# Performance work log

Measured on AMD Instinct MI355X. Metric: run time of the kernel, lower is better.

Reference implementation:

```python
import jax, jax.numpy as jnp
import numpy as np

EPS = 1e-5


def _bn_relu(h, gamma, beta):
    # BatchNorm1d in training mode: stats over all but the last (channel) dim
    m = h.reshape(-1, h.shape[-1])
    mu = jnp.mean(m, axis=0)
    var = jnp.var(m, axis=0)
    return jax.nn.relu((h - mu) * jax.lax.rsqrt(var + EPS) * gamma + beta)


def setup_inputs() -> dict:
    key = jax.random.key(0)
    ks = jax.random.split(key, 16)
    B, N, D, OUT = 64, 64, 64, 128
    T = 2 * D          # object_tuple_size = 128
    HG, HF = 256, 128  # hidden_dim_g, hidden_dim_f

    def lin(k, i, o):
        return (jax.random.normal(k, (i, o), jnp.float32) / np.sqrt(i).astype(np.float32),
                jnp.zeros((o,), jnp.float32))

    inp = {"x": jax.random.normal(ks[0], (B, N, D), jnp.float32)}
    # G: depth-3 Linear-BN-ReLU, dims T -> HG -> HG -> T
    for i, (a, b) in enumerate([(T, HG), (HG, HG), (HG, T)]):
        W, bb = lin(ks[1 + i], a, b)
        inp[f"gW{i}"] = W
        inp[f"gb{i}"] = bb
        inp[f"gg{i}"] = jnp.ones((b,), jnp.float32)
        inp[f"gB{i}"] = jnp.zeros((b,), jnp.float32)
    # F: depth-2 Linear-BN-ReLU, dims T -> HF -> T, then Linear(T, OUT)
    for i, (a, b) in enumerate([(T, HF), (HF, T)]):
        W, bb = lin(ks[5 + i], a, b)
        inp[f"fW{i}"] = W
        inp[f"fb{i}"] = bb
        inp[f"fg{i}"] = jnp.ones((b,), jnp.float32)
        inp[f"fB{i}"] = jnp.zeros((b,), jnp.float32)
    inp["foW"], inp["fob"] = lin(ks[8], T, OUT)
    return inp


def reference(x, gW0, gb0, gg0, gB0, gW1, gb1, gg1, gB1, gW2, gb2, gg2, gB2,
              fW0, fb0, fg0, fB0, fW1, fb1, fg1, fB1, foW, fob):
    B, N, D = x.shape
    # GroupObjectsIntoPairs: all ordered pairs -> (B, N*N, 2D)
    xi = jnp.broadcast_to(x[:, :, None, :], (B, N, N, D))
    xj = jnp.broadcast_to(x[:, None, :, :], (B, N, N, D))
    h = jnp.concatenate([xi, xj], axis=-1).reshape(B, N * N, 2 * D)
    # G: per-pair MLP
    for W, b, g, be in ((gW0, gb0, gg0, gB0), (gW1, gb1, gg1, gB1), (gW2, gb2, gg2, gB2)):
        h = _bn_relu(h @ W + b, g, be)
    # sum over pair dimension (no layer norm)
    s = h.sum(axis=1)  # (B, 2D)
    # F: MLP + final linear
    for W, b, g, be in ((fW0, fb0, fg0, fB0), (fW1, fb1, fg1, fB1)):
        s = _bn_relu(s @ W + b, g, be)
    return s @ foW + fob  # (B, OUT)
```

## Files before the change

### kernel.cpp

```cpp
#include <hip/hip_runtime.h>


typedef _Float16 half8 __attribute__((ext_vector_type(8)));
typedef _Float16 half4_t __attribute__((ext_vector_type(4)));
typedef float float4_t __attribute__((ext_vector_type(4)));

static constexpr float kEps = 1e-5f;
static constexpr float kM = 262144.f;

static constexpr size_t OFF_U   = 0;
static constexpr size_t OFF_V   = OFF_U  + (size_t)4096*256*4;
static constexpr size_t OFF_UP  = OFF_V  + (size_t)4096*256*4;
static constexpr size_t OFF_VP  = OFF_UP + (size_t)4096*256*2;
static constexpr size_t OFF_W1T = OFF_VP + (size_t)4096*256*2;
static constexpr size_t OFF_W2T = OFF_W1T + (size_t)256*256*2;
static constexpr size_t OFF_Z1  = OFF_W2T + (size_t)128*256*2;
static constexpr size_t OFF_ST0 = OFF_Z1 + (size_t)262144*256*2;
static constexpr size_t OFF_C0S = OFF_ST0 + (size_t)64*4*256*4;
static constexpr size_t OFF_C0T = OFF_C0S + 1024;
static constexpr size_t OFF_C1S = OFF_C0T + 1024;
static constexpr size_t OFF_C1T = OFF_C1S + 1024;
static constexpr size_t OFF_C2S = OFF_C1T + 1024;
static constexpr size_t OFF_C2T = OFF_C2S + 512;
static constexpr size_t OFF_ST1 = OFF_C2T + 512;
static constexpr size_t OFF_ST2 = OFF_ST1 + (size_t)32*512*4;
static constexpr size_t OFF_SB  = OFF_ST2 + (size_t)32*256*4;
static constexpr size_t OFF_FST0 = OFF_SB + (size_t)64*128*4;
static constexpr size_t OFF_FST1 = OFF_FST0 + 1024;
static constexpr size_t ZERO_BYTES = (size_t)32*512*4 + (size_t)32*256*4
                                   + (size_t)64*128*4 + 2048;
static constexpr size_t OFF_FZ0  = OFF_FST1 + 1024;
static constexpr size_t OFF_FZ1  = OFF_FZ0 + (size_t)64*128*4;
static constexpr size_t OFF_CF0S = OFF_FZ1 + (size_t)64*128*4;
static constexpr size_t OFF_CF0T = OFF_CF0S + 512;
static constexpr size_t OFF_CF1S = OFF_CF0T + 512;
static constexpr size_t OFF_CF1T = OFF_CF1S + 512;
static constexpr size_t OFF_C1H  = OFF_CF1T + 512;
static constexpr size_t OFF_Z2   = OFF_C1H + 1024;
static constexpr size_t WS_REQUIRED = OFF_Z2 + (size_t)262144*128*2;

static __device__ inline half8 relu8(half8 s) {
#pragma unroll
  for (int e = 0; e < 8; ++e) s[e] = s[e] > (_Float16)0 ? s[e] : (_Float16)0;
  return s;
}

__global__ __launch_bounds__(256) void k_wt(const float* __restrict__ gW1,
                                            const float* __restrict__ gW2,
                                            _Float16* __restrict__ W1T,
                                            _Float16* __restrict__ W2T) {
  int idx = blockIdx.x * 256 + threadIdx.x;
  if (idx < 65536) {
    int n = idx >> 8, k = idx & 255;
    W1T[idx] = (_Float16)gW1[k * 256 + n];
  } else if (idx < 98304) {
    int j = idx - 65536;
    int n = j >> 8, k = j & 255;
    W2T[j] = (_Float16)gW2[k * 128 + n];
  }
}

__global__ __launch_bounds__(256) void k_prep(const float* __restrict__ x,
                                              const float* __restrict__ gW0,
                                              float* __restrict__ U,
                                              float* __restrict__ V) {
  __shared__ __align__(16) float sX[32 * 64];
  int t = threadIdx.x;
  int p0 = blockIdx.x * 32;
  int by = blockIdx.y;
  int hsel = by >> 1;
  int cbase = (by & 1) * 128;
#pragma unroll
  for (int it = 0; it < 2; ++it) {
    int f4 = (it * 256 + t) * 4;
    *(float4_t*)(sX + f4) = *(const float4_t*)(x + (size_t)p0 * 64 + f4);
  }
  __syncthreads();
  int r = t >> 3, cg = (t & 7) * 16;
  const float* Wb = gW0 + (size_t)(hsel * 64) * 256 + cbase + cg;
  float acc[16];
#pragma unroll
  for (int j = 0; j < 16; ++j) acc[j] = 0.f;
  for (int k = 0; k < 64; ++k) {
    float xv = sX[r * 64 + k];
    const float4_t* wr = (const float4_t*)(Wb + (size_t)k * 256);
    float4_t w0 = wr[0], w1 = wr[1], w2 = wr[2], w3 = wr[3];
#pragma unroll
    for (int j = 0; j < 4; ++j) {
      acc[j]      += xv * w0[j];
      acc[4 + j]  += xv * w1[j];
      acc[8 + j]  += xv * w2[j];
      acc[12 + j] += xv * w3[j];
    }
  }
  float* outp = (hsel ? V : U) + (size_t)(p0 + r) * 256 + cbase + cg;
#pragma unroll
  for (int q = 0; q < 4; ++q) {
    float4_t o = {acc[q * 4], acc[q * 4 + 1], acc[q * 4 + 2], acc[q * 4 + 3]};
    *(float4_t*)(outp + q * 4) = o;
  }
}

__global__ __launch_bounds__(256) void k_stats0(const float* __restrict__ U,
                                                const float* __restrict__ V,
                                                float* __restrict__ st0) {
  int b = blockIdx.x, c = threadIdx.x;
  float su = 0, su2 = 0, sv = 0, sv2 = 0;
  for (int i = 0; i < 64; ++i) {
    float u = U[(size_t)(b * 64 + i) * 256 + c];
    float v = V[(size_t)(b * 64 + i) * 256 + c];
    su += u; su2 += u * u; sv += v; sv2 += v * v;
  }
  st0[(b * 4 + 0) * 256 + c] = su;
  st0[(b * 4 + 1) * 256 + c] = su2;
  st0[(b * 4 + 2) * 256 + c] = sv;
  st0[(b * 4 + 3) * 256 + c] = sv2;
}

__global__ __launch_bounds__(256) void k_bn0(const float* __restrict__ st0,
                                             const float* __restrict__ gb0,
                                             const float* __restrict__ gg0,
                                             const float* __restrict__ gB0,
                                             float* __restrict__ c0s,
                                             float* __restrict__ c0t) {
  int c = threadIdx.x;
  float su = 0, su2 = 0, sv = 0, sv2 = 0, cross = 0;
  for (int b = 0; b < 64; ++b) {
    float a  = st0[(b * 4 + 0) * 256 + c];
    float a2 = st0[(b * 4 + 1) * 256 + c];
    float v  = st0[(b * 4 + 2) * 256 + c];
    float v2 = st0[(b * 4 + 3) * 256 + c];
    su += a; su2 += a2; sv += v; sv2 += v2; cross += a * v;
  }
  float b0 = gb0[c];
  float sumz  = 64.f * (su + sv) + kM * b0;
  float sumzz = 64.f * (su2 + sv2) + 2.f * cross + 2.f * b0 * 64.f * (su + sv) + kM * b0 * b0;
  float mu = sumz / kM;
  float var = sumzz / kM - mu * mu;
  float sc = gg0[c] * rsqrtf(var + kEps);
  c0s[c] = sc;
  c0t[c] = gB0[c] + sc * (b0 - mu);
}

__global__ __launch_bounds__(256) void k_uv(const float* __restrict__ U,
                                            const float* __restrict__ V,
                                            const float* __restrict__ c0s,
                                            const float* __restrict__ c0t,
                                            _Float16* __restrict__ Up,
                                            _Float16* __restrict__ Vp) {
  int idx = blockIdx.x * 256 + threadIdx.x;
  int e4 = idx * 4;
  int c4 = e4 & 255;
  float4_t u = *(const float4_t*)(U + e4);
  float4_t v = *(const float4_t*)(V + e4);
  float4_t s = *(const float4_t*)(c0s + c4);
  float4_t tt = *(const float4_t*)(c0t + c4);
  half4_t hu, hv;
#pragma unroll
  for (int e = 0; e < 4; ++e) {
    hu[e] = (_Float16)(u[e] * s[e] + tt[e]);
    hv[e] = (_Float16)(v[e] * s[e]);
  }
  *(half4_t*)(Up + e4) = hu;
  *(half4_t*)(Vp + e4) = hv;
}

__global__ __launch_bounds__(256) void k_gemm1(const _Float16* __restrict__ Up,
                                               const _Float16* __restrict__ Vp,
                                               const _Float16* __restrict__ W1T,
                                               const float* __restrict__ gb1,
                                               _Float16* __restrict__ Z1,
                                               float* __restrict__ stats1) {
  __shared__ __align__(16) char smem[2 * 128 * 72 * 2];
  _Float16* sA = (_Float16*)smem;
  _Float16* sW = (_Float16*)(smem + 128 * 72 * 2);
  _Float16* sO = (_Float16*)smem;

  const int t = threadIdx.x;
  const int bx = blockIdx.x;
  const int n0 = blockIdx.y * 128;
  const int b = bx >> 5;
  const int i0 = (bx & 31) * 2;
  const long R0 = (long)bx * 128;

  const int wid = t >> 6, L = t & 63;
  const int wrow = wid >> 1, wcol = wid & 1;
  const int quad = L >> 4, l15 = L & 15;

  const int prow = t >> 2;
  const int pk = (t & 3) * 16;

  const _Float16* UpI0 = Up + (size_t)(b * 64 + i0) * 256;
  const _Float16* UpI1 = UpI0 + 256;
  const _Float16* VpJ  = Vp + (size_t)(b * 64 + prow) * 256;

  float4_t acc[4][4];
#pragma unroll
  for (int mt = 0; mt < 4; ++mt)
#pragma unroll
    for (int nt = 0; nt < 4; ++nt) acc[mt][nt] = (float4_t){0.f, 0.f, 0.f, 0.f};

  for (int kc = 0; kc < 4; ++kc) {
    __syncthreads();
    {
      const int kg = kc * 64 + pk;
      half8 va = *(const half8*)(VpJ + kg);
      half8 vb = *(const half8*)(VpJ + kg + 8);
      half8 u0a = *(const half8*)(UpI0 + kg);
      half8 u0b = *(const half8*)(UpI0 + kg + 8);
      half8 u1a = *(const half8*)(UpI1 + kg);
      half8 u1b = *(const half8*)(UpI1 + kg + 8);
      *(half8*)(sA + prow * 72 + pk)            = relu8(u0a + va);
      *(half8*)(sA + prow * 72 + pk + 8)        = relu8(u0b + vb);
      *(half8*)(sA + (64 + prow) * 72 + pk)     = relu8(u1a + va);
      *(half8*)(sA + (64 + prow) * 72 + pk + 8) = relu8(u1b + vb);
    }
#pragma unroll
    for (int it = 0; it < 4; ++it) {
      int flat = it * 256 + t;
      int row = flat >> 3, c8 = (flat & 7) * 8;
      *(half8*)(sW + row * 72 + c8) =
          *(const half8*)(W1T + (size_t)(n0 + row) * 256 + kc * 64 + c8);
    }
    __syncthreads();
#pragma unroll
    for (int ks = 0; ks < 2; ++ks) {
      const int kk = ks * 32 + quad * 8;
      half8 afr[4];
#pragma unroll
      for (int mt = 0; mt < 4; ++mt)
        afr[mt] = *(const half8*)(sA + (wrow * 64 + mt * 16 + l15) * 72 + kk);
      half8 bfr[4];
#pragma unroll
      for (int nt = 0; nt < 4; ++nt)
        bfr[nt] = *(const half8*)(sW + (wcol * 64 + nt * 16 + l15) * 72 + kk);
#pragma unroll
      for (int mt = 0; mt < 4; ++mt)
#pragma unroll
        for (int nt = 0; nt < 4; ++nt)
          acc[mt][nt] = __builtin_amdgcn_mfma_f32_16x16x32_f16(afr[mt], bfr[nt],
                                                               acc[mt][nt], 0, 0, 0);
    }
  }

  __syncthreads();
  const int rep = bx & 31;
#pragma unroll
  for (int nt = 0; nt < 4; ++nt) {
    const int lcol = wcol * 64 + nt * 16 + l15;
    const float b1c = gb1[n0 + lcol];
    float sz = 0.f, szz = 0.f;
#pragma unroll
    for (int mt = 0; mt < 4; ++mt) {
      const int lrow = wrow * 64 + mt * 16 + quad * 4;
#pragma unroll
      for (int r = 0; r < 4; ++r) {
        float z = acc[mt][nt][r] + b1c;
        sO[(lrow + r) * 136 + lcol] = (_Float16)z;
        sz += z;
        szz += z * z;
      }
    }
    sz += __shfl_xor(sz, 16, 64);
    sz += __shfl_xor(sz, 32, 64);
    szz += __shfl_xor(szz, 16, 64);
    szz += __shfl_xor(szz, 32, 64);
    if (quad == 0) {
      atomicAdd(stats1 + rep * 512 + n0 + lcol, sz);
      atomicAdd(stats1 + rep * 512 + 256 + n0 + lcol, szz);
    }
  }
  __syncthreads();
#pragma unroll
  for (int it = 0; it < 8; ++it) {
    int cid = it * 256 + t;
    int row = cid >> 4, ch = (cid & 15) * 8;
    half8 hv = *(const half8*)(sO + row * 136 + ch);
    *(half8*)(Z1 + (size_t)(R0 + row) * 256 + n0 + ch) = hv;
  }
}

__global__ __launch_bounds__(256) void k_bn1(const float* __restrict__ stats1,
                                             const float* __restrict__ gg1,
                                             const float* __restrict__ gB1,
                                             float* __restrict__ c1s,
                                             float* __restrict__ c1t,
                                             _Float16* __restrict__ c1h) {
  int c = threadIdx.x;
  float S = 0.f, S2 = 0.f;
  for (int rp = 0; rp < 32; ++rp) {
    S += stats1[rp * 512 + c];
    S2 += stats1[rp * 512 + 256 + c];
  }
  float mu = S / kM;
  float var = S2 / kM - mu * mu;
  float sc = gg1[c] * rsqrtf(var + kEps);
  float sh = gB1[c] - sc * mu;
  c1s[c] = sc;
  c1t[c] = sh;
  c1h[c] = (_Float16)sc;
  c1h[256 + c] = (_Float16)sh;
}

__global__ __launch_bounds__(256) void k_gemm2(const _Float16* __restrict__ Z1,
                                               const _Float16* __restrict__ W2T,
                                               const _Float16* __restrict__ c1h,
                                               const float* __restrict__ gb2,
                                               _Float16* __restrict__ Z2,
                                               float* __restrict__ stats2) {
  __shared__ __align__(16) char smem[2 * 128 * 72 * 2];
  _Float16* sA = (_Float16*)smem;
  _Float16* sW = (_Float16*)(smem + 128 * 72 * 2);
  _Float16* sO = (_Float16*)smem;
  __shared__ __align__(16) _Float16 sSh[256];
  __shared__ __align__(16) _Float16 sTh[256];
  const int t = threadIdx.x;
  const int bx = blockIdx.x;
  const long R0 = (long)bx * 128;
  sSh[t] = c1h[t];
  sTh[t] = c1h[256 + t];

  const int wid = t >> 6, L = t & 63;
  const int wrow = wid >> 1, wcol = wid & 1;
  const int quad = L >> 4, l15 = L & 15;

  float4_t acc[4][4];
#pragma unroll
  for (int mt = 0; mt < 4; ++mt)
#pragma unroll
    for (int nt = 0; nt < 4; ++nt) acc[mt][nt] = (float4_t){0.f, 0.f, 0.f, 0.f};

  for (int kc = 0; kc < 4; ++kc) {
    __syncthreads();
#pragma unroll
    for (int it = 0; it < 2; ++it) {
      int flat = it * 256 + t;
      int row = flat >> 3, k8 = (flat & 7) * 8;
      int kg = kc * 64 + k8;
      half8 hv = *(const half8*)(Z1 + ((size_t)R0 + row) * 256 + kg);
      half8 hs = *(const half8*)(sSh + kg);
      half8 ht = *(const half8*)(sTh + kg);
      half8 ov = relu8(hv * hs + ht);
      *(half8*)(sA + row * 72 + k8) = ov;
      int row2 = row + 64;
      half8 hv2 = *(const half8*)(Z1 + ((size_t)R0 + row2) * 256 + kg);
      half8 ov2 = relu8(hv2 * hs + ht);
      *(half8*)(sA + row2 * 72 + k8) = ov2;
    }
#pragma unroll
    for (int it = 0; it < 4; ++it) {
      int flat = it * 256 + t;
      int row = flat >> 3, k8 = (flat & 7) * 8;
      *(half8*)(sW + row * 72 + k8) =
          *(const half8*)(W2T + (size_t)row * 256 + kc * 64 + k8);
    }
    __syncthreads();
#pragma unroll
    for (int ks = 0; ks < 2; ++ks) {
      const int kk = ks * 32 + quad * 8;
      half8 afr[4];
#pragma unroll
      for (int mt = 0; mt < 4; ++mt)
        afr[mt] = *(const half8*)(sA + (wrow * 64 + mt * 16 + l15) * 72 + kk);
      half8 bfr[4];
#pragma unroll
      for (int nt = 0; nt < 4; ++nt)
        bfr[nt] = *(const half8*)(sW + (wcol * 64 + nt * 16 + l15) * 72 + kk);
#pragma unroll
      for (int mt = 0; mt < 4; ++mt)
#pragma unroll
        for (int nt = 0; nt < 4; ++nt)
          acc[mt][nt] = __builtin_amdgcn_mfma_f32_16x16x32_f16(afr[mt], bfr[nt],
                                                               acc[mt][nt], 0, 0, 0);
    }
  }

  __syncthreads();
  const int rep = bx & 31;
#pragma unroll
  for (int nt = 0; nt < 4; ++nt) {
    const int lcol = wcol * 64 + nt * 16 + l15;
    const float b2c = gb2[lcol];
    float sz = 0.f, szz = 0.f;
#pragma unroll
    for (int mt = 0; mt < 4; ++mt) {
      const int lrow = wrow * 64 + mt * 16 + quad * 4;
#pragma unroll
      for (int r = 0; r < 4; ++r) {
        float z = acc[mt][nt][r] + b2c;
        sO[(lrow + r) * 136 + lcol] = (_Float16)z;
        sz += z;
        szz += z * z;
      }
    }
    sz += __shfl_xor(sz, 16, 64);
    sz += __shfl_xor(sz, 32, 64);
    szz += __shfl_xor(szz, 16, 64);
    szz += __shfl_xor(szz, 32, 64);
    if (quad == 0) {
      atomicAdd(stats2 + rep * 256 + lcol, sz);
      atomicAdd(stats2 + rep * 256 + 128 + lcol, szz);
    }
  }
  __syncthreads();
#pragma unroll
  for (int it = 0; it < 8; ++it) {
    int cid = it * 256 + t;
    int row = cid >> 4, ch = (cid & 15) * 8;
    half8 hv = *(const half8*)(sO + row * 136 + ch);
    *(half8*)(Z2 + (size_t)(R0 + row) * 128 + ch) = hv;
  }
}

template <int FINAL>
__global__ __launch_bounds__(256) void k_gemm23(const _Float16* __restrict__ Z1,
                                                const _Float16* __restrict__ W2T,
                                                const float* __restrict__ c1s,
                                                const float* __restrict__ c1t,
                                                const float* __restrict__ gb2,
                                                const float* __restrict__ c2s,
                                                const float* __restrict__ c2t,
                                                float* __restrict__ stats2,
                                                float* __restrict__ sbuf) {
  __shared__ __align__(16) _Float16 sA[128 * 72];
  __shared__ __align__(16) _Float16 sW[128 * 72];
  __shared__ __align__(16) float sS[256];
  __shared__ __align__(16) float sT[256];
  const int t = threadIdx.x;
  const int bx = blockIdx.x;
  const long R0 = (long)bx * 128;
  sS[t] = c1s[t];
  sT[t] = c1t[t];

  const int wid = t >> 6, L = t & 63;
  const int wrow = wid >> 1, wcol = wid & 1;
  const int quad = L >> 4, l15 = L & 15;

  float4_t acc[4][4];
#pragma unroll
  for (int mt = 0; mt < 4; ++mt)
#pragma unroll
    for (int nt = 0; nt < 4; ++nt) acc[mt][nt] = (float4_t){0.f, 0.f, 0.f, 0.f};

  for (int kc = 0; kc < 4; ++kc) {
    __syncthreads();
#pragma unroll
    for (int it = 0; it < 4; ++it) {
      int flat = it * 256 + t;
      int row = flat >> 3, k8 = (flat & 7) * 8;
      int kg = kc * 64 + k8;
      half8 hv = *(const half8*)(Z1 + ((size_t)R0 + row) * 256 + kg);
      float4_t s0 = *(const float4_t*)(sS + kg);
      float4_t s1 = *(const float4_t*)(sS + kg + 4);
      float4_t t0 = *(const float4_t*)(sT + kg);
      float4_t t1 = *(const float4_t*)(sT + kg + 4);
      half8 ov;
#pragma unroll
      for (int e = 0; e < 4; ++e) {
        ov[e]     = (_Float16)fmaxf(s0[e] * (float)hv[e] + t0[e], 0.f);
        ov[4 + e] = (_Float16)fmaxf(s1[e] * (float)hv[4 + e] + t1[e], 0.f);
      }
      *(half8*)(sA + row * 72 + k8) = ov;
    }
#pragma unroll
    for (int it = 0; it < 4; ++it) {
      int flat = it * 256 + t;
      int n = flat >> 3, k8 = (flat & 7) * 8;
      *(half8*)(sW + n * 72 + k8) =
          *(const half8*)(W2T + (size_t)n * 256 + kc * 64 + k8);
    }
    __syncthreads();
#pragma unroll
    for (int ks = 0; ks < 2; ++ks) {
      const int kk = ks * 32 + quad * 8;
      half8 afr[4];
#pragma unroll
      for (int mt = 0; mt < 4; ++mt)
        afr[mt] = *(const half8*)(sA + (wrow * 64 + mt * 16 + l15) * 72 + kk);
      half8 bfr[4];
#pragma unroll
      for (int nt = 0; nt < 4; ++nt)
        bfr[nt] = *(const half8*)(sW + (wcol * 64 + nt * 16 + l15) * 72 + kk);
#pragma unroll
      for (int mt = 0; mt < 4; ++mt)
#pragma unroll
        for (int nt = 0; nt < 4; ++nt)
          acc[mt][nt] = __builtin_amdgcn_mfma_f32_16x16x32_f16(afr[mt], bfr[nt],
                                                               acc[mt][nt], 0, 0, 0);
    }
  }

  const int rep = bx & 31;
#pragma unroll
  for (int nt = 0; nt < 4; ++nt) {
    const int col = wcol * 64 + nt * 16 + l15;
    const float b2c = gb2[col];
    if (FINAL) {
      const float s2 = c2s[col], t2 = c2t[col];
      float ps = 0.f;
#pragma unroll
      for (int mt = 0; mt < 4; ++mt)
#pragma unroll
        for (int r = 0; r < 4; ++r)
          ps += fmaxf(s2 * (acc[mt][nt][r] + b2c) + t2, 0.f);
      ps += __shfl_xor(ps, 16, 64);
      ps += __shfl_xor(ps, 32, 64);
      if (quad == 0) atomicAdd(sbuf + (bx >> 5) * 128 + col, ps);
    } else {
      float sz = 0.f, szz = 0.f;
#pragma unroll
      for (int mt = 0; mt < 4; ++mt)
#pragma unroll
        for (int r = 0; r < 4; ++r) {
          float z = acc[mt][nt][r] + b2c;
          sz += z;
          szz += z * z;
        }
      sz += __shfl_xor(sz, 16, 64);
      sz += __shfl_xor(sz, 32, 64);
      szz += __shfl_xor(szz, 16, 64);
      szz += __shfl_xor(szz, 32, 64);
      if (quad == 0) {
        atomicAdd(stats2 + rep * 256 + col, sz);
        atomicAdd(stats2 + rep * 256 + 128 + col, szz);
      }
    }
  }
}

__global__ __launch_bounds__(128) void k_bn2(const float* __restrict__ stats2,
                                             const float* __restrict__ gg2,
                                             const float* __restrict__ gB2,
                                             float* __restrict__ c2s,
                                             float* __restrict__ c2t) {
  int c = threadIdx.x;
  float S = 0.f, S2 = 0.f;
  for (int rp = 0; rp < 32; ++rp) {
    S += stats2[rp * 256 + c];
    S2 += stats2[rp * 256 + 128 + c];
  }
  float mu = S / kM;
  float var = S2 / kM - mu * mu;
  float sc = gg2[c] * rsqrtf(var + kEps);
  c2s[c] = sc;
  c2t[c] = gB2[c] - sc * mu;
}

__global__ __launch_bounds__(256) void k_red(const _Float16* __restrict__ Z2,
                                             const float* __restrict__ c2s,
                                             const float* __restrict__ c2t,
                                             float* __restrict__ sbuf) {
  __shared__ float sR[256 * 8];
  const int t = threadIdx.x;
  const int bx = blockIdx.x;
  const int b = bx >> 5;
  const long row0 = (long)bx * 128;
  const int rr = t >> 4;
  const int c8 = (t & 15) * 8;

  float4_t s0 = *(const float4_t*)(c2s + c8);
  float4_t s1 = *(const float4_t*)(c2s + c8 + 4);
  float4_t t0 = *(const float4_t*)(c2t + c8);
  float4_t t1 = *(const float4_t*)(c2t + c8 + 4);

  float acc[8];
#pragma unroll
  for (int e = 0; e < 8; ++e) acc[e] = 0.f;
#pragma unroll
  for (int it = 0; it < 8; ++it) {
    long row = row0 + it * 16 + rr;
    half8 h = *(const half8*)(Z2 + row * 128 + c8);
#pragma unroll
    for (int e = 0; e < 4; ++e) {
      acc[e]     += fmaxf(s0[e] * (float)h[e] + t0[e], 0.f);
      acc[4 + e] += fmaxf(s1[e] * (float)h[4 + e] + t1[e], 0.f);
    }
  }
#pragma unroll
  for (int e = 0; e < 8; ++e) sR[t * 8 + e] = acc[e];
  __syncthreads();
  if (t < 128) {
    float S = 0.f;
#pragma unroll
    for (int rr2 = 0; rr2 < 16; ++rr2) S += sR[rr2 * 128 + t];
    atomicAdd(sbuf + b * 128 + t, S);
  }
}

template <bool APPLY_BN, bool STATS>
__global__ __launch_bounds__(256) void k_fg(const float* __restrict__ in,
                                            const float* __restrict__ cs,
                                            const float* __restrict__ ct,
                                            const float* __restrict__ W,
                                            const float* __restrict__ bias,
                                            float* __restrict__ zout,
                                            float* __restrict__ stats) {
  __shared__ __align__(16) float sIn[8 * 128];
  __shared__ __align__(16) float sZ[8 * 128];
  const int t = threadIdx.x;
  const int r0 = blockIdx.x * 8;
  {
    int flat = t * 4;
    int col = flat & 127;
    float4_t v = *(const float4_t*)(in + (size_t)r0 * 128 + flat);
    if (APPLY_BN) {
      float4_t s = *(const float4_t*)(cs + col);
      float4_t sh = *(const float4_t*)(ct + col);
#pragma unroll
      for (int e = 0; e < 4; ++e) v[e] = fmaxf(s[e] * v[e] + sh[e], 0.f);
    }
    *(float4_t*)(sIn + flat) = v;
  }
  __syncthreads();

  const int r = t >> 5;
  const int c4 = (t & 31) * 4;
  float4_t acc = *(const float4_t*)(bias + c4);
  for (int k = 0; k < 128; ++k) {
    float xv = sIn[r * 128 + k];
    float4_t w = *(const float4_t*)(W + (size_t)k * 128 + c4);
#pragma unroll
    for (int e = 0; e < 4; ++e) acc[e] += xv * w[e];
  }
  *(float4_t*)(zout + (size_t)(r0 + r) * 128 + c4) = acc;

  if (STATS) {
    *(float4_t*)(sZ + r * 128 + c4) = acc;
    __syncthreads();
    if (t < 128) {
      float S = 0.f, S2 = 0.f;
#pragma unroll
      for (int rr = 0; rr < 8; ++rr) {
        float z = sZ[rr * 128 + t];
        S += z;
        S2 += z * z;
      }
      atomicAdd(stats + t, S);
      atomicAdd(stats + 128 + t, S2);
    }
  }
}

__global__ __launch_bounds__(128) void k_fbn(const float* __restrict__ stats,
                                             const float* __restrict__ g,
                                             const float* __restrict__ B,
                                             float* __restrict__ cs,
                                             float* __restrict__ ct) {
  int c = threadIdx.x;
  float S = stats[c], S2 = stats[128 + c];
  float mu = S / 64.f;
  float var = S2 / 64.f - mu * mu;
  float sc = g[c] * rsqrtf(var + kEps);
  cs[c] = sc;
  ct[c] = B[c] - sc * mu;
}

extern "C" void kernel_launch(void* const* d_in, const int* in_sizes, int n_in,
                              void* d_out, int out_size, void* d_ws, size_t ws_size,
                              hipStream_t stream) {
  (void)in_sizes; (void)n_in; (void)out_size;
  const float* x   = (const float*)d_in[0];
  const float* gW0 = (const float*)d_in[1];
  const float* gb0 = (const float*)d_in[2];
  const float* gg0 = (const float*)d_in[3];
  const float* gB0 = (const float*)d_in[4];
  const float* gW1 = (const float*)d_in[5];
  const float* gb1 = (const float*)d_in[6];
  const float* gg1 = (const float*)d_in[7];
  const float* gB1 = (const float*)d_in[8];
  const float* gW2 = (const float*)d_in[9];
  const float* gb2 = (const float*)d_in[10];
  const float* gg2 = (const float*)d_in[11];
  const float* gB2 = (const float*)d_in[12];
  const float* fW0 = (const float*)d_in[13];
  const float* fb0 = (const float*)d_in[14];
  const float* fg0 = (const float*)d_in[15];
  const float* fB0 = (const float*)d_in[16];
  const float* fW1 = (const float*)d_in[17];
  const float* fb1 = (const float*)d_in[18];
  const float* fg1 = (const float*)d_in[19];
  const float* fB1 = (const float*)d_in[20];
  const float* foW = (const float*)d_in[21];
  const float* fob = (const float*)d_in[22];
  float* out = (float*)d_out;

  char* ws = (char*)d_ws;
  float*    U    = (float*)(ws + OFF_U);
  float*    V    = (float*)(ws + OFF_V);
  _Float16* Up   = (_Float16*)(ws + OFF_UP);
  _Float16* Vp   = (_Float16*)(ws + OFF_VP);
  _Float16* W1T  = (_Float16*)(ws + OFF_W1T);
  _Float16* W2T  = (_Float16*)(ws + OFF_W2T);
  _Float16* Z1   = (_Float16*)(ws + OFF_Z1);
  float*    st0  = (float*)(ws + OFF_ST0);
  float*    c0s  = (float*)(ws + OFF_C0S);
  float*    c0t  = (float*)(ws + OFF_C0T);
  float*    c1s  = (float*)(ws + OFF_C1S);
  float*    c1t  = (float*)(ws + OFF_C1T);
  float*    c2s  = (float*)(ws + OFF_C2S);
  float*    c2t  = (float*)(ws + OFF_C2T);
  float*    st1  = (float*)(ws + OFF_ST1);
  float*    st2  = (float*)(ws + OFF_ST2);
  float*    sbuf = (float*)(ws + OFF_SB);
  float*    fst0 = (float*)(ws + OFF_FST0);
  float*    fst1 = (float*)(ws + OFF_FST1);
  float*    fz0  = (float*)(ws + OFF_FZ0);
  float*    fz1  = (float*)(ws + OFF_FZ1);
  float*    cf0s = (float*)(ws + OFF_CF0S);
  float*    cf0t = (float*)(ws + OFF_CF0T);
  float*    cf1s = (float*)(ws + OFF_CF1S);
  float*    cf1t = (float*)(ws + OFF_CF1T);
  _Float16* c1h  = (_Float16*)(ws + OFF_C1H);
  _Float16* Z2   = (_Float16*)(ws + OFF_Z2);

  hipMemsetAsync(ws + OFF_ST1, 0, ZERO_BYTES, stream);

  k_wt<<<384, 256, 0, stream>>>(gW1, gW2, W1T, W2T);
  k_prep<<<dim3(128, 4), 256, 0, stream>>>(x, gW0, U, V);
  k_stats0<<<64, 256, 0, stream>>>(U, V, st0);
  k_bn0<<<1, 256, 0, stream>>>(st0, gb0, gg0, gB0, c0s, c0t);
  k_uv<<<1024, 256, 0, stream>>>(U, V, c0s, c0t, Up, Vp);
  k_gemm1<<<dim3(2048, 2), 256, 0, stream>>>(Up, Vp, W1T, gb1, Z1, st1);
  k_bn1<<<1, 256, 0, stream>>>(st1, gg1, gB1, c1s, c1t, c1h);

  if (ws_size >= WS_REQUIRED) {
    k_gemm2<<<2048, 256, 0, stream>>>(Z1, W2T, c1h, gb2, Z2, st2);
    k_bn2<<<1, 128, 0, stream>>>(st2, gg2, gB2, c2s, c2t);
    k_red<<<2048, 256, 0, stream>>>(Z2, c2s, c2t, sbuf);
  } else {
    k_gemm23<0><<<2048, 256, 0, stream>>>(Z1, W2T, c1s, c1t, gb2, c2s, c2t, st2, sbuf);
    k_bn2<<<1, 128, 0, stream>>>(st2, gg2, gB2, c2s, c2t);
    k_gemm23<1><<<2048, 256, 0, stream>>>(Z1, W2T, c1s, c1t, gb2, c2s, c2t, st2, sbuf);
  }

  k_fg<false, true><<<8, 256, 0, stream>>>(sbuf, nullptr, nullptr, fW0, fb0, fz0, fst0);
  k_fbn<<<1, 128, 0, stream>>>(fst0, fg0, fB0, cf0s, cf0t);
  k_fg<true, true><<<8, 256, 0, stream>>>(fz0, cf0s, cf0t, fW1, fb1, fz1, fst1);
  k_fbn<<<1, 128, 0, stream>>>(fst1, fg1, fB1, cf1s, cf1t);
  k_fg<true, false><<<8, 256, 0, stream>>>(fz1, cf1s, cf1t, foW, fob, out, nullptr);
}
```

Before: 302.9 us.

## Fold BN finalize kernels into consumers and drop memset via in-kernel zeroing

Removes the single-block BN finalize kernels (k_bn1, k_bn2, k_fbn) and the k_stats0 kernel. Each consumer block now recomputes the per-channel scale and shift from the raw partial statistics, and k_prep accumulates layer-0 statistics through shared memory and atomics. The hipMemsetAsync is replaced by zeroing inside k_wt. This cuts about seven launches and their serialization bubbles, at the cost of redundant per-block statistics reads (32x2 loads per thread across 2048 blocks) and extra atomics in k_prep.

```diff
diff --git a/kernel.cpp b/kernel.cpp
--- a/kernel.cpp
+++ b/kernel.cpp
@@ -15,28 +15,18 @@
 static constexpr size_t OFF_W1T = OFF_VP + (size_t)4096*256*2;
 static constexpr size_t OFF_W2T = OFF_W1T + (size_t)256*256*2;
 static constexpr size_t OFF_Z1  = OFF_W2T + (size_t)128*256*2;
-static constexpr size_t OFF_ST0 = OFF_Z1 + (size_t)262144*256*2;
-static constexpr size_t OFF_C0S = OFF_ST0 + (size_t)64*4*256*4;
+static constexpr size_t OFF_C0S = OFF_Z1 + (size_t)262144*256*2;
 static constexpr size_t OFF_C0T = OFF_C0S + 1024;
-static constexpr size_t OFF_C1S = OFF_C0T + 1024;
-static constexpr size_t OFF_C1T = OFF_C1S + 1024;
-static constexpr size_t OFF_C2S = OFF_C1T + 1024;
-static constexpr size_t OFF_C2T = OFF_C2S + 512;
-static constexpr size_t OFF_ST1 = OFF_C2T + 512;
+static constexpr size_t OFF_ST0 = OFF_C0T + 1024;
+static constexpr size_t OFF_ST1 = OFF_ST0 + (size_t)64*4*256*4;
 static constexpr size_t OFF_ST2 = OFF_ST1 + (size_t)32*512*4;
 static constexpr size_t OFF_SB  = OFF_ST2 + (size_t)32*256*4;
 static constexpr size_t OFF_FST0 = OFF_SB + (size_t)64*128*4;
 static constexpr size_t OFF_FST1 = OFF_FST0 + 1024;
-static constexpr size_t ZERO_BYTES = (size_t)32*512*4 + (size_t)32*256*4
-                                   + (size_t)64*128*4 + 2048;
+static constexpr int ZERO_FLOATS = (64*4*256 + 32*512 + 32*256 + 64*128 + 256 + 256);
 static constexpr size_t OFF_FZ0  = OFF_FST1 + 1024;
 static constexpr size_t OFF_FZ1  = OFF_FZ0 + (size_t)64*128*4;
-static constexpr size_t OFF_CF0S = OFF_FZ1 + (size_t)64*128*4;
-static constexpr size_t OFF_CF0T = OFF_CF0S + 512;
-static constexpr size_t OFF_CF1S = OFF_CF0T + 512;
-static constexpr size_t OFF_CF1T = OFF_CF1S + 512;
-static constexpr size_t OFF_C1H  = OFF_CF1T + 512;
-static constexpr size_t OFF_Z2   = OFF_C1H + 1024;
+static constexpr size_t OFF_Z2   = OFF_FZ1 + (size_t)64*128*4;
 static constexpr size_t WS_REQUIRED = OFF_Z2 + (size_t)262144*128*2;
 
 static __device__ inline half8 relu8(half8 s) {
@@ -48,7 +38,8 @@
 __global__ __launch_bounds__(256) void k_wt(const float* __restrict__ gW1,
                                             const float* __restrict__ gW2,
                                             _Float16* __restrict__ W1T,
-                                            _Float16* __restrict__ W2T) {
+                                            _Float16* __restrict__ W2T,
+                                            float* __restrict__ zbuf) {
   int idx = blockIdx.x * 256 + threadIdx.x;
   if (idx < 65536) {
     int n = idx >> 8, k = idx & 255;
@@ -58,13 +49,16 @@
     int n = j >> 8, k = j & 255;
     W2T[j] = (_Float16)gW2[k * 128 + n];
   }
+  if (idx < ZERO_FLOATS) zbuf[idx] = 0.f;
 }
 
 __global__ __launch_bounds__(256) void k_prep(const float* __restrict__ x,
                                               const float* __restrict__ gW0,
                                               float* __restrict__ U,
-                                              float* __restrict__ V) {
+                                              float* __restrict__ V,
+                                              float* __restrict__ st0) {
   __shared__ __align__(16) float sX[32 * 64];
+  __shared__ __align__(16) float sZ[32 * 128];
   int t = threadIdx.x;
   int p0 = blockIdx.x * 32;
   int by = blockIdx.y;
@@ -99,22 +93,21 @@
     float4_t o = {acc[q * 4], acc[q * 4 + 1], acc[q * 4 + 2], acc[q * 4 + 3]};
     *(float4_t*)(outp + q * 4) = o;
   }
-}
-
-__global__ __launch_bounds__(256) void k_stats0(const float* __restrict__ U,
-                                                const float* __restrict__ V,
-                                                float* __restrict__ st0) {
-  int b = blockIdx.x, c = threadIdx.x;
-  float su = 0, su2 = 0, sv = 0, sv2 = 0;
-  for (int i = 0; i < 64; ++i) {
-    float u = U[(size_t)(b * 64 + i) * 256 + c];
-    float v = V[(size_t)(b * 64 + i) * 256 + c];
-    su += u; su2 += u * u; sv += v; sv2 += v * v;
-  }
-  st0[(b * 4 + 0) * 256 + c] = su;
-  st0[(b * 4 + 1) * 256 + c] = su2;
-  st0[(b * 4 + 2) * 256 + c] = sv;
-  st0[(b * 4 + 3) * 256 + c] = sv2;
+#pragma unroll
+  for (int j = 0; j < 16; ++j) sZ[r * 128 + cg + j] = acc[j];
+  __syncthreads();
+  if (t < 128) {
+    float S = 0.f, S2 = 0.f;
+#pragma unroll
+    for (int rr = 0; rr < 32; ++rr) {
+      float z = sZ[rr * 128 + t];
+      S += z;
+      S2 += z * z;
+    }
+    int b = blockIdx.x >> 1;
+    atomicAdd(st0 + (size_t)(b * 4 + hsel * 2 + 0) * 256 + cbase + t, S);
+    atomicAdd(st0 + (size_t)(b * 4 + hsel * 2 + 1) * 256 + cbase + t, S2);
+  }
 }
 
 __global__ __launch_bounds__(256) void k_bn0(const float* __restrict__ st0,
@@ -280,31 +273,11 @@
   }
 }
 
-__global__ __launch_bounds__(256) void k_bn1(const float* __restrict__ stats1,
-                                             const float* __restrict__ gg1,
-                                             const float* __restrict__ gB1,
-                                             float* __restrict__ c1s,
-                                             float* __restrict__ c1t,
-                                             _Float16* __restrict__ c1h) {
-  int c = threadIdx.x;
-  float S = 0.f, S2 = 0.f;
-  for (int rp = 0; rp < 32; ++rp) {
-    S += stats1[rp * 512 + c];
-    S2 += stats1[rp * 512 + 256 + c];
-  }
-  float mu = S / kM;
-  float var = S2 / kM - mu * mu;
-  float sc = gg1[c] * rsqrtf(var + kEps);
-  float sh = gB1[c] - sc * mu;
-  c1s[c] = sc;
-  c1t[c] = sh;
-  c1h[c] = (_Float16)sc;
-  c1h[256 + c] = (_Float16)sh;
-}
-
 __global__ __launch_bounds__(256) void k_gemm2(const _Float16* __restrict__ Z1,
                                                const _Float16* __restrict__ W2T,
-                                               const _Float16* __restrict__ c1h,
+                                               const float* __restrict__ st1,
+                                               const float* __restrict__ gg1,
+                                               const float* __restrict__ gB1,
                                                const float* __restrict__ gb2,
                                                _Float16* __restrict__ Z2,
                                                float* __restrict__ stats2) {
@@ -317,8 +290,20 @@
   const int t = threadIdx.x;
   const int bx = blockIdx.x;
   const long R0 = (long)bx * 128;
-  sSh[t] = c1h[t];
-  sTh[t] = c1h[256 + t];
+
+  {
+    float S = 0.f, S2 = 0.f;
+#pragma unroll
+    for (int rp = 0; rp < 32; ++rp) {
+      S += st1[rp * 512 + t];
+      S2 += st1[rp * 512 + 256 + t];
+    }
+    float mu = S / kM;
+    float var = S2 / kM - mu * mu;
+    float sc = gg1[t] * rsqrtf(var + kEps);
+    sSh[t] = (_Float16)sc;
+    sTh[t] = (_Float16)(gB1[t] - sc * mu);
+  }
 
   const int wid = t >> 6, L = t & 63;
   const int wrow = wid >> 1, wcol = wid & 1;
@@ -337,15 +322,13 @@
       int flat = it * 256 + t;
       int row = flat >> 3, k8 = (flat & 7) * 8;
       int kg = kc * 64 + k8;
-      half8 hv = *(const half8*)(Z1 + ((size_t)R0 + row) * 256 + kg);
       half8 hs = *(const half8*)(sSh + kg);
       half8 ht = *(const half8*)(sTh + kg);
-      half8 ov = relu8(hv * hs + ht);
-      *(half8*)(sA + row * 72 + k8) = ov;
+      half8 hv = *(const half8*)(Z1 + ((size_t)R0 + row) * 256 + kg);
+      *(half8*)(sA + row * 72 + k8) = relu8(hv * hs + ht);
       int row2 = row + 64;
       half8 hv2 = *(const half8*)(Z1 + ((size_t)R0 + row2) * 256 + kg);
-      half8 ov2 = relu8(hv2 * hs + ht);
-      *(half8*)(sA + row2 * 72 + k8) = ov2;
+      *(half8*)(sA + row2 * 72 + k8) = relu8(hv2 * hs + ht);
     }
 #pragma unroll
     for (int it = 0; it < 4; ++it) {
@@ -415,22 +398,51 @@
 template <int FINAL>
 __global__ __launch_bounds__(256) void k_gemm23(const _Float16* __restrict__ Z1,
                                                 const _Float16* __restrict__ W2T,
-                                                const float* __restrict__ c1s,
-                                                const float* __restrict__ c1t,
+                                                const float* __restrict__ st1,
+                                                const float* __restrict__ gg1,
+                                                const float* __restrict__ gB1,
                                                 const float* __restrict__ gb2,
-                                                const float* __restrict__ c2s,
-                                                const float* __restrict__ c2t,
+                                                const float* __restrict__ st2,
+                                                const float* __restrict__ gg2,
+                                                const float* __restrict__ gB2,
                                                 float* __restrict__ stats2,
                                                 float* __restrict__ sbuf) {
   __shared__ __align__(16) _Float16 sA[128 * 72];
   __shared__ __align__(16) _Float16 sW[128 * 72];
-  __shared__ __align__(16) float sS[256];
-  __shared__ __align__(16) float sT[256];
+  __shared__ __align__(16) _Float16 sSh[256];
+  __shared__ __align__(16) _Float16 sTh[256];
+  __shared__ __align__(16) float sS2[128];
+  __shared__ __align__(16) float sT2[128];
   const int t = threadIdx.x;
   const int bx = blockIdx.x;
   const long R0 = (long)bx * 128;
-  sS[t] = c1s[t];
-  sT[t] = c1t[t];
+
+  {
+    float S = 0.f, S2 = 0.f;
+#pragma unroll
+    for (int rp = 0; rp < 32; ++rp) {
+      S += st1[rp * 512 + t];
+      S2 += st1[rp * 512 + 256 + t];
+    }
+    float mu = S / kM;
+    float var = S2 / kM - mu * mu;
+    float sc = gg1[t] * rsqrtf(var + kEps);
+    sSh[t] = (_Float16)sc;
+    sTh[t] = (_Float16)(gB1[t] - sc * mu);
+  }
+  if (FINAL && t < 128) {
+    float S = 0.f, S2 = 0.f;
+#pragma unroll
+    for (int rp = 0; rp < 32; ++rp) {
+      S += st2[rp * 256 + t];
+      S2 += st2[rp * 256 + 128 + t];
+    }
+    float mu = S / kM;
+    float var = S2 / kM - mu * mu;
+    float sc = gg2[t] * rsqrtf(var + kEps);
+    sS2[t] = sc;
+    sT2[t] = gB2[t] - sc * mu;
+  }
 
   const int wid = t >> 6, L = t & 63;
   const int wrow = wid >> 1, wcol = wid & 1;
@@ -445,22 +457,17 @@
   for (int kc = 0; kc < 4; ++kc) {
     __syncthreads();
 #pragma unroll
-    for (int it = 0; it < 4; ++it) {
+    for (int it = 0; it < 2; ++it) {
       int flat = it * 256 + t;
       int row = flat >> 3, k8 = (flat & 7) * 8;
       int kg = kc * 64 + k8;
+      half8 hs = *(const half8*)(sSh + kg);
+      half8 ht = *(const half8*)(sTh + kg);
       half8 hv = *(const half8*)(Z1 + ((size_t)R0 + row) * 256 + kg);
-      float4_t s0 = *(const float4_t*)(sS + kg);
-      float4_t s1 = *(const float4_t*)(sS + kg + 4);
-      float4_t t0 = *(const float4_t*)(sT + kg);
-      float4_t t1 = *(const float4_t*)(sT + kg + 4);
-      half8 ov;
-#pragma unroll
-      for (int e = 0; e < 4; ++e) {
-        ov[e]     = (_Float16)fmaxf(s0[e] * (float)hv[e] + t0[e], 0.f);
-        ov[4 + e] = (_Float16)fmaxf(s1[e] * (float)hv[4 + e] + t1[e], 0.f);
-      }
-      *(half8*)(sA + row * 72 + k8) = ov;
+      *(half8*)(sA + row * 72 + k8) = relu8(hv * hs + ht);
+      int row2 = row + 64;
+      half8 hv2 = *(const half8*)(Z1 + ((size_t)R0 + row2) * 256 + kg);
+      *(half8*)(sA + row2 * 72 + k8) = relu8(hv2 * hs + ht);
     }
 #pragma unroll
     for (int it = 0; it < 4; ++it) {
@@ -496,7 +503,7 @@
     const int col = wcol * 64 + nt * 16 + l15;
     const float b2c = gb2[col];
     if (FINAL) {
-      const float s2 = c2s[col], t2 = c2t[col];
+      const float s2 = sS2[col], t2 = sT2[col];
       float ps = 0.f;
 #pragma unroll
       for (int mt = 0; mt < 4; ++mt)
@@ -528,40 +535,40 @@
   }
 }
 
-__global__ __launch_bounds__(128) void k_bn2(const float* __restrict__ stats2,
+__global__ __launch_bounds__(256) void k_red(const _Float16* __restrict__ Z2,
+                                             const float* __restrict__ st2,
                                              const float* __restrict__ gg2,
                                              const float* __restrict__ gB2,
-                                             float* __restrict__ c2s,
-                                             float* __restrict__ c2t) {
-  int c = threadIdx.x;
-  float S = 0.f, S2 = 0.f;
-  for (int rp = 0; rp < 32; ++rp) {
-    S += stats2[rp * 256 + c];
-    S2 += stats2[rp * 256 + 128 + c];
-  }
-  float mu = S / kM;
-  float var = S2 / kM - mu * mu;
-  float sc = gg2[c] * rsqrtf(var + kEps);
-  c2s[c] = sc;
-  c2t[c] = gB2[c] - sc * mu;
-}
-
-__global__ __launch_bounds__(256) void k_red(const _Float16* __restrict__ Z2,
-                                             const float* __restrict__ c2s,
-                                             const float* __restrict__ c2t,
                                              float* __restrict__ sbuf) {
   __shared__ float sR[256 * 8];
+  __shared__ __align__(16) float sS2[128];
+  __shared__ __align__(16) float sT2[128];
   const int t = threadIdx.x;
   const int bx = blockIdx.x;
   const int b = bx >> 5;
   const long row0 = (long)bx * 128;
+
+  if (t < 128) {
+    float S = 0.f, S2 = 0.f;
+#pragma unroll
+    for (int rp = 0; rp < 32; ++rp) {
+      S += st2[rp * 256 + t];
+      S2 += st2[rp * 256 + 128 + t];
+    }
+    float mu = S / kM;
+    float var = S2 / kM - mu * mu;
+    float sc = gg2[t] * rsqrtf(var + kEps);
+    sS2[t] = sc;
+    sT2[t] = gB2[t] - sc * mu;
+  }
+  __syncthreads();
+
   const int rr = t >> 4;
   const int c8 = (t & 15) * 8;
-
-  float4_t s0 = *(const float4_t*)(c2s + c8);
-  float4_t s1 = *(const float4_t*)(c2s + c8 + 4);
-  float4_t t0 = *(const float4_t*)(c2t + c8);
-  float4_t t1 = *(const float4_t*)(c2t + c8 + 4);
+  float4_t s0 = *(const float4_t*)(sS2 + c8);
+  float4_t s1 = *(const float4_t*)(sS2 + c8 + 4);
+  float4_t t0 = *(const float4_t*)(sT2 + c8);
+  float4_t t1 = *(const float4_t*)(sT2 + c8 + 4);
 
   float acc[8];
 #pragma unroll
@@ -589,23 +596,38 @@
 
 template <bool APPLY_BN, bool STATS>
 __global__ __launch_bounds__(256) void k_fg(const float* __restrict__ in,
-                                            const float* __restrict__ cs,
-                                            const float* __restrict__ ct,
+                                            const float* __restrict__ prevStats,
+                                            const float* __restrict__ g,
+                                            const float* __restrict__ B,
                                             const float* __restrict__ W,
                                             const float* __restrict__ bias,
                                             float* __restrict__ zout,
                                             float* __restrict__ stats) {
   __shared__ __align__(16) float sIn[8 * 128];
   __shared__ __align__(16) float sZ[8 * 128];
+  __shared__ __align__(16) float sCs[128];
+  __shared__ __align__(16) float sCt[128];
   const int t = threadIdx.x;
   const int r0 = blockIdx.x * 8;
+
+  if (APPLY_BN) {
+    if (t < 128) {
+      float S = prevStats[t], S2 = prevStats[128 + t];
+      float mu = S / 64.f;
+      float var = S2 / 64.f - mu * mu;
+      float sc = g[t] * rsqrtf(var + kEps);
+      sCs[t] = sc;
+      sCt[t] = B[t] - sc * mu;
+    }
+    __syncthreads();
+  }
   {
     int flat = t * 4;
     int col = flat & 127;
     float4_t v = *(const float4_t*)(in + (size_t)r0 * 128 + flat);
     if (APPLY_BN) {
-      float4_t s = *(const float4_t*)(cs + col);
-      float4_t sh = *(const float4_t*)(ct + col);
+      float4_t s = *(const float4_t*)(sCs + col);
+      float4_t sh = *(const float4_t*)(sCt + col);
 #pragma unroll
       for (int e = 0; e < 4; ++e) v[e] = fmaxf(s[e] * v[e] + sh[e], 0.f);
     }
@@ -639,20 +661,6 @@
       atomicAdd(stats + 128 + t, S2);
     }
   }
-}
-
-__global__ __launch_bounds__(128) void k_fbn(const float* __restrict__ stats,
-                                             const float* __restrict__ g,
-                                             const float* __restrict__ B,
-                                             float* __restrict__ cs,
-                                             float* __restrict__ ct) {
-  int c = threadIdx.x;
-  float S = stats[c], S2 = stats[128 + c];
-  float mu = S / 64.f;
-  float var = S2 / 64.f - mu * mu;
-  float sc = g[c] * rsqrtf(var + kEps);
-  cs[c] = sc;
-  ct[c] = B[c] - sc * mu;
 }
 
 extern "C" void kernel_launch(void* const* d_in, const int* in_sizes, int n_in,
@@ -692,13 +700,9 @@
   _Float16* W1T  = (_Float16*)(ws + OFF_W1T);
   _Float16* W2T  = (_Float16*)(ws + OFF_W2T);
   _Float16* Z1   = (_Float16*)(ws + OFF_Z1);
-  float*    st0  = (float*)(ws + OFF_ST0);
   float*    c0s  = (float*)(ws + OFF_C0S);
   float*    c0t  = (float*)(ws + OFF_C0T);
-  float*    c1s  = (float*)(ws + OFF_C1S);
-  float*    c1t  = (float*)(ws + OFF_C1T);
-  float*    c2s  = (float*)(ws + OFF_C2S);
-  float*    c2t  = (float*)(ws + OFF_C2T);
+  float*    st0  = (float*)(ws + OFF_ST0);
   float*    st1  = (float*)(ws + OFF_ST1);
   float*    st2  = (float*)(ws + OFF_ST2);
   float*    sbuf = (float*)(ws + OFF_SB);
@@ -706,36 +710,28 @@
   float*    fst1 = (float*)(ws + OFF_FST1);
   float*    fz0  = (float*)(ws + OFF_FZ0);
   float*    fz1  = (float*)(ws + OFF_FZ1);
-  float*    cf0s = (float*)(ws + OFF_CF0S);
-  float*    cf0t = (float*)(ws + OFF_CF0T);
-  float*    cf1s = (float*)(ws + OFF_CF1S);
-  float*    cf1t = (float*)(ws + OFF_CF1T);
-  _Float16* c1h  = (_Float16*)(ws + OFF_C1H);
   _Float16* Z2   = (_Float16*)(ws + OFF_Z2);
 
-  hipMemsetAsync(ws + OFF_ST1, 0, ZERO_BYTES, stream);
-
-  k_wt<<<384, 256, 0, stream>>>(gW1, gW2, W1T, W2T);
-  k_prep<<<dim3(128, 4), 256, 0, stream>>>(x, gW0, U, V);
-  k_stats0<<<64, 256, 0, stream>>>(U, V, st0);
+  k_wt<<<386, 256, 0, stream>>>(gW1, gW2, W1T, W2T, st0);
+  k_prep<<<dim3(128, 4), 256, 0, stream>>>(x, gW0, U, V, st0);
   k_bn0<<<1, 256, 0, stream>>>(st0, gb0, gg0, gB0, c0s, c0t);
   k_uv<<<1024, 256, 0, stream>>>(U, V, c0s, c0t, Up, Vp);
   k_gemm1<<<dim3(2048, 2), 256, 0, stream>>>(Up, Vp, W1T, gb1, Z1, st1);
-  k_bn1<<<1, 256, 0, stream>>>(st1, gg1, gB1, c1s, c1t, c1h);
 
   if (ws_size >= WS_REQUIRED) {
-    k_gemm2<<<2048, 256, 0, stream>>>(Z1, W2T, c1h, gb2, Z2, st2);
-    k_bn2<<<1, 128, 0, stream>>>(st2, gg2, gB2, c2s, c2t);
-    k_red<<<2048, 256, 0, stream>>>(Z2, c2s, c2t, sbuf);
+    k_gemm2<<<2048, 256, 0, stream>>>(Z1, W2T, st1, gg1, gB1, gb2, Z2, st2);
+    k_red<<<2048, 256, 0, stream>>>(Z2, st2, gg2, gB2, sbuf);
   } else {
-    k_gemm23<0><<<2048, 256, 0, stream>>>(Z1, W2T, c1s, c1t, gb2, c2s, c2t, st2, sbuf);
-    k_bn2<<<1, 128, 0, stream>>>(st2, gg2, gB2, c2s, c2t);
-    k_gemm23<1><<<2048, 256, 0, stream>>>(Z1, W2T, c1s, c1t, gb2, c2s, c2t, st2, sbuf);
-  }
-
-  k_fg<false, true><<<8, 256, 0, stream>>>(sbuf, nullptr, nullptr, fW0, fb0, fz0, fst0);
-  k_fbn<<<1, 128, 0, stream>>>(fst0, fg0, fB0, cf0s, cf0t);
-  k_fg<true, true><<<8, 256, 0, stream>>>(fz0, cf0s, cf0t, fW1, fb1, fz1, fst1);
-  k_fbn<<<1, 128, 0, stream>>>(fst1, fg1, fB1, cf1s, cf1t);
-  k_fg<true, false><<<8, 256, 0, stream>>>(fz1, cf1s, cf1t, foW, fob, out, nullptr);
-}
+    k_gemm23<0><<<2048, 256, 0, stream>>>(Z1, W2T, st1, gg1, gB1, gb2,
+                                          st2, gg2, gB2, st2, sbuf);
+    k_gemm23<1><<<2048, 256, 0, stream>>>(Z1, W2T, st1, gg1, gB1, gb2,
+                                          st2, gg2, gB2, st2, sbuf);
+  }
+
+  k_fg<false, true><<<8, 256, 0, stream>>>(sbuf, nullptr, nullptr, nullptr,
+                                           fW0, fb0, fz0, fst0);
+  k_fg<true, true><<<8, 256, 0, stream>>>(fz0, fst0, fg0, fB0,
+                                          fW1, fb1, fz1, fst1);
+  k_fg<true, false><<<8, 256, 0, stream>>>(fz1, fst1, fg1, fB1,
+                                           foW, fob, out, nullptr);
+}
```

Result: faster. 285.9 us (-5.6%).
